# Performance work log

Measured on AMD Instinct MI355X. Metric: run time of the kernel, lower is better.

Reference implementation:

```python
import jax, jax.numpy as jnp
import numpy as np
import math

D_MODEL = 512
NHEAD = 8
N_LAYERS = 3
D_FF = 2048
INPUT_DIM = 128
NUM_CLASSES = 64
FACTOR = 5


def setup_inputs() -> dict:
    key = jax.random.key(0)
    ks = jax.random.split(key, 24)
    s = 0.02
    d, f, nl = D_MODEL, D_FF, N_LAYERS
    inp = {
        "x": jax.random.normal(ks[0], (4, 1024, INPUT_DIM), dtype=jnp.float32),
        "W_emb": jax.random.normal(ks[1], (INPUT_DIM, d), dtype=jnp.float32) * s,
        "b_emb": jnp.zeros((d,), jnp.float32),
        "Wq": jax.random.normal(ks[2], (nl, d, d), dtype=jnp.float32) * s,
        "bq": jnp.zeros((nl, d), jnp.float32),
        "Wk": jax.random.normal(ks[3], (nl, d, d), dtype=jnp.float32) * s,
        "bk": jnp.zeros((nl, d), jnp.float32),
        "Wv": jax.random.normal(ks[4], (nl, d, d), dtype=jnp.float32) * s,
        "bv": jnp.zeros((nl, d), jnp.float32),
        "Wo": jax.random.normal(ks[5], (nl, d, d), dtype=jnp.float32) * s,
        "bo": jnp.zeros((nl, d), jnp.float32),
        "ln1_g": jnp.ones((nl, d), jnp.float32),
        "ln1_b": jnp.zeros((nl, d), jnp.float32),
        "W1": jax.random.normal(ks[6], (nl, d, f), dtype=jnp.float32) * s,
        "b1": jnp.zeros((nl, f), jnp.float32),
        "W2": jax.random.normal(ks[7], (nl, f, d), dtype=jnp.float32) * s,
        "b2": jnp.zeros((nl, d), jnp.float32),
        "ln2_g": jnp.ones((nl, d), jnp.float32),
        "ln2_b": jnp.zeros((nl, d), jnp.float32),
        "W_dec": jax.random.normal(ks[8], (d, NUM_CLASSES), dtype=jnp.float32) * s,
        "b_dec": jnp.zeros((NUM_CLASSES,), jnp.float32),
    }
    return inp


def _layer_norm(x, g, b, eps=1e-5):
    m = jnp.mean(x, axis=-1, keepdims=True)
    v = jnp.var(x, axis=-1, keepdims=True)
    return (x - m) * jax.lax.rsqrt(v + eps) * g + b


def _pos_encoding(L, d):
    pos = jnp.arange(L, dtype=jnp.float32)[:, None]
    div = jnp.exp(jnp.arange(0, d, 2, dtype=jnp.float32) * (-math.log(10000.0) / d))
    pe = jnp.zeros((L, d), jnp.float32)
    pe = pe.at[:, 0::2].set(jnp.sin(pos * div))
    pe = pe.at[:, 1::2].set(jnp.cos(pos * div))
    return pe


def _prob_sparse_attn(x, Wq, bq, Wk, bk, Wv, bv, Wo, bo):
    B, L, d = x.shape
    H, dk = NHEAD, d // NHEAD
    u = min(L, int(FACTOR * math.log(L)) if L > 1 else L)
    Q = (x @ Wq + bq).reshape(B, L, H, dk).transpose(0, 2, 1, 3)  # bhld
    K = (x @ Wk + bk).reshape(B, L, H, dk).transpose(0, 2, 1, 3)
    V = (x @ Wv + bv).reshape(B, L, H, dk).transpose(0, 2, 1, 3)
    scores = jnp.einsum("bhld,bhmd->bhlm", Q, K) / math.sqrt(dk)  # [B,H,L,L]
    kth = jax.lax.top_k(scores, u)[0][..., -1:]  # kth-largest per row
    scores = jnp.where(scores < kth, -10000.0, scores)
    attn = jax.nn.softmax(scores, axis=-1)
    out = jnp.einsum("bhlm,bhmd->bhld", attn, V)
    out = out.transpose(0, 2, 1, 3).reshape(B, L, d)
    return out @ Wo + bo


def reference(x, W_emb, b_emb, Wq, bq, Wk, bk, Wv, bv, Wo, bo,
              ln1_g, ln1_b, W1, b1, W2, b2, ln2_g, ln2_b, W_dec, b_dec):
    B, L, _ = x.shape
    h = (x @ W_emb + b_emb) * math.sqrt(D_MODEL)
    h = h + _pos_encoding(L, D_MODEL)[None]
    for i in range(N_LAYERS):
        a = _prob_sparse_attn(h, Wq[i], bq[i], Wk[i], bk[i], Wv[i], bv[i], Wo[i], bo[i])
        h = _layer_norm(h + a, ln1_g[i], ln1_b[i])
        ff = jax.nn.relu(h @ W1[i] + b1[i]) @ W2[i] + b2[i]
        h = _layer_norm(h + ff, ln2_g[i], ln2_b[i])
    return h @ W_dec + b_dec
```

## Files before the change

### kernel.cpp

```cpp
#include <hip/hip_runtime.h>
#include <math.h>

#define SEQ 1024
#define BATCH 4
#define DMODEL 512
#define NHEAD 8
#define DK 64
#define DFF 2048
#define U_TOP 34
#define ROWS (BATCH * SEQ)

typedef unsigned short ushort_t;
typedef __attribute__((ext_vector_type(8))) short short8;
typedef __attribute__((ext_vector_type(4))) float float4v;

__device__ inline ushort_t f2bf(float f) {
  unsigned u = __float_as_uint(f);
  unsigned r = u + 0x7fffu + ((u >> 16) & 1u);
  return (ushort_t)(r >> 16);
}
__device__ inline float bf2f(ushort_t u) {
  return __uint_as_float((unsigned)u << 16);
}
__device__ inline float keyinv(unsigned cand) {
  unsigned fb = (cand & 0x80000000u) ? (cand ^ 0x80000000u) : ~cand;
  return __uint_as_float(fb);
}

union H16 { _Float16 h; unsigned short u; };
__device__ inline unsigned short h2u(float f) {
  H16 t; t.h = (_Float16)f; return t.u;
}
__device__ inline float u2h(unsigned short u) {
  H16 t; t.u = u; return (float)t.h;
}
__device__ inline int mbcnt64(unsigned long long m) {
  int lo = __builtin_amdgcn_mbcnt_lo((unsigned)m, 0);
  return __builtin_amdgcn_mbcnt_hi((unsigned)(m >> 32), lo);
}

__device__ inline void glds16(const void* g, void* l) {
  __builtin_amdgcn_global_load_lds(
      (const __attribute__((address_space(1))) unsigned int*)g,
      (__attribute__((address_space(3))) unsigned int*)l, 16, 0, 0);
}

__device__ inline void bitonic64x2(float& a, float& b, int lane) {
#pragma unroll
  for (int k = 2; k <= 64; k <<= 1) {
#pragma unroll
    for (int j = k >> 1; j > 0; j >>= 1) {
      float pa = __shfl_xor(a, j);
      float pb = __shfl_xor(b, j);
      bool keepMin = (((lane & k) != 0) == ((lane & j) == 0));
      a = keepMin ? fminf(a, pa) : fmaxf(a, pa);
      b = keepMin ? fminf(b, pb) : fmaxf(b, pb);
    }
  }
}

template <int RELU, int SPLIT>
__global__ __launch_bounds__(256) void gemm128(
    const ushort_t* __restrict__ A, const short* __restrict__ Bt,
    const float* __restrict__ b0, const float* __restrict__ b1,
    const float* __restrict__ b2, ushort_t* __restrict__ Cout,
    int K, int N, int zCstride) {
  __shared__ short As[128 * 32];
  __shared__ short Bs[128 * 32];

  const int tid = threadIdx.x;
  const int lane = tid & 63, w = tid >> 6;
  const int wm = w >> 1, wn = w & 1;
  const int quad = lane >> 4, r16 = lane & 15;
  const int bm = blockIdx.y * 128, bn = blockIdx.x * 128;

  const int srow = lane >> 2, skseg = lane & 3;
  const ushort_t* Ag0 = A + (size_t)(bm + w * 16 + srow) * K + skseg * 8;
  const ushort_t* Ag1 = Ag0 + (size_t)64 * K;
  const short* Bg0 = Bt + (size_t)(bn + w * 16 + srow) * K + skseg * 8;
  const short* Bg1 = Bg0 + (size_t)64 * K;
  short* lA0 = As + (w * 16) * 32;
  short* lA1 = As + (64 + w * 16) * 32;
  short* lB0 = Bs + (w * 16) * 32;
  short* lB1 = Bs + (64 + w * 16) * 32;

  float4v acc[4][4];
#pragma unroll
  for (int m = 0; m < 4; ++m)
#pragma unroll
    for (int n = 0; n < 4; ++n) acc[m][n] = (float4v){0.f, 0.f, 0.f, 0.f};

  for (int k0 = 0; k0 < K; k0 += 32) {
    __syncthreads();
    glds16(Ag0 + k0, lA0);
    glds16(Ag1 + k0, lA1);
    glds16(Bg0 + k0, lB0);
    glds16(Bg1 + k0, lB1);
    __syncthreads();

    short8 af[4], bfr[4];
#pragma unroll
    for (int m = 0; m < 4; ++m)
      af[m] = *(const short8*)&As[(wm * 64 + m * 16 + r16) * 32 + quad * 8];
#pragma unroll
    for (int n = 0; n < 4; ++n)
      bfr[n] = *(const short8*)&Bs[(wn * 64 + n * 16 + r16) * 32 + quad * 8];
#pragma unroll
    for (int m = 0; m < 4; ++m)
#pragma unroll
      for (int n = 0; n < 4; ++n)
        acc[m][n] = __builtin_amdgcn_mfma_f32_16x16x32_bf16(af[m], bfr[n],
                                                            acc[m][n], 0, 0, 0);
  }

  const int z = SPLIT ? (bn >> 9) : 0;
  const float* bias = (z == 0) ? b0 : (z == 1 ? b1 : b2);
  const int cbase = SPLIT ? (bn & 511) : bn;
  const int strideN = SPLIT ? 512 : N;
  ushort_t* C = Cout + (SPLIT ? (size_t)z * zCstride : (size_t)0);

  float bias_n[4];
#pragma unroll
  for (int n = 0; n < 4; ++n)
    bias_n[n] = bias[cbase + wn * 64 + n * 16 + r16];

#pragma unroll
  for (int m = 0; m < 4; ++m) {
#pragma unroll
    for (int n = 0; n < 4; ++n) {
      int col = cbase + wn * 64 + n * 16 + r16;
#pragma unroll
      for (int reg = 0; reg < 4; ++reg) {
        int row = bm + wm * 64 + m * 16 + quad * 4 + reg;
        float v = acc[m][n][reg] + bias_n[n];
        if (RELU) v = fmaxf(v, 0.f);
        C[(size_t)row * strideN + col] = f2bf(v);
      }
    }
  }
}

template <int RELU, int OUTBF16, int EPI, int ADDC>
__global__ __launch_bounds__(256) void gemm64(
    const ushort_t* __restrict__ A, const short* __restrict__ Bt,
    const float* __restrict__ bias, void* __restrict__ Cout,
    const ushort_t* __restrict__ Cadd, int K, int N) {
  __shared__ short As[64 * 32];
  __shared__ short Bs[64 * 32];

  const int tid = threadIdx.x;
  const int lane = tid & 63, w = tid >> 6;
  const int wm = w >> 1, wn = w & 1;
  const int quad = lane >> 4, r16 = lane & 15;
  const int bm = blockIdx.y * 64, bn = blockIdx.x * 64;

  const int srow = tid >> 2, skseg = tid & 3;
  const ushort_t* Ag = A + (size_t)(bm + srow) * K + skseg * 8;
  const short* Bg = Bt + (size_t)(bn + srow) * K + skseg * 8;
  short* lA = As + w * 512;
  short* lB = Bs + w * 512;

  float4v acc[2][2];
#pragma unroll
  for (int m = 0; m < 2; ++m)
#pragma unroll
    for (int n = 0; n < 2; ++n) acc[m][n] = (float4v){0.f, 0.f, 0.f, 0.f};

  for (int k0 = 0; k0 < K; k0 += 32) {
    __syncthreads();
    glds16(Ag + k0, lA);
    glds16(Bg + k0, lB);
    __syncthreads();

    short8 af[2], bfr[2];
#pragma unroll
    for (int m = 0; m < 2; ++m)
      af[m] = *(const short8*)&As[(wm * 32 + m * 16 + r16) * 32 + quad * 8];
#pragma unroll
    for (int n = 0; n < 2; ++n)
      bfr[n] = *(const short8*)&Bs[(wn * 32 + n * 16 + r16) * 32 + quad * 8];
#pragma unroll
    for (int m = 0; m < 2; ++m)
#pragma unroll
      for (int n = 0; n < 2; ++n)
        acc[m][n] = __builtin_amdgcn_mfma_f32_16x16x32_bf16(af[m], bfr[n],
                                                            acc[m][n], 0, 0, 0);
  }

  const float pe_c = (float)(-9.210340371976184 / 512.0);
  const float sqrtd = 22.62741699796952f;

  float bias_n[2];
#pragma unroll
  for (int n = 0; n < 2; ++n) bias_n[n] = bias[bn + wn * 32 + n * 16 + r16];

#pragma unroll
  for (int m = 0; m < 2; ++m) {
#pragma unroll
    for (int n = 0; n < 2; ++n) {
      int col = bn + wn * 32 + n * 16 + r16;
#pragma unroll
      for (int reg = 0; reg < 4; ++reg) {
        int row = bm + wm * 32 + m * 16 + quad * 4 + reg;
        float v = acc[m][n][reg] + bias_n[n];
        if (RELU) v = fmaxf(v, 0.f);
        if (EPI == 2) {
          int pos = row & (SEQ - 1);
          float e = __expf((float)(col & ~1) * pe_c);
          float arg = (float)pos * e;
          v = v * sqrtd + ((col & 1) ? __cosf(arg) : __sinf(arg));
        }
        if (ADDC) v += bf2f(Cadd[(size_t)row * N + col]);
        if (OUTBF16) {
          ((ushort_t*)Cout)[(size_t)row * N + col] = f2bf(v);
        } else {
          ((float*)Cout)[(size_t)row * N + col] = v;
        }
      }
    }
  }
}

__global__ __launch_bounds__(256) void convert_all(
    const float* __restrict__ Wq, const float* __restrict__ Wk,
    const float* __restrict__ Wv, const float* __restrict__ Wo,
    const float* __restrict__ W1, const float* __restrict__ W2,
    const float* __restrict__ W_emb, const float* __restrict__ W_dec,
    short* __restrict__ wt) {
  __shared__ float t[32][33];
  int id = blockIdx.x;
  const float* src;
  short* dst;
  int K, N, tk, tn;
  if (id < 9216) {
    int lay = id / 3072, r = id % 3072;
    short* wl = wt + (size_t)lay * 3145728;
    const size_t wsz = 512 * 512;
    if (r < 1024) {
      int wi = r >> 8, tile = r & 255;
      const float* base = (wi == 0) ? Wq : (wi == 1) ? Wk : (wi == 2) ? Wv : Wo;
      src = base + lay * wsz;
      dst = wl + wi * 262144;
      K = 512; N = 512; tk = tile >> 4; tn = tile & 15;
    } else if (r < 2048) {
      int tile = r - 1024;
      src = W1 + (size_t)lay * 512 * 2048;
      dst = wl + 1048576;
      K = 512; N = 2048; tk = tile >> 6; tn = tile & 63;
    } else {
      int tile = r - 2048;
      src = W2 + (size_t)lay * 2048 * 512;
      dst = wl + 2097152;
      K = 2048; N = 512; tk = tile >> 4; tn = tile & 15;
    }
  } else {
    int r = id - 9216;
    if (r < 64) {
      src = W_emb; dst = wt + 9437184; K = 128; N = 512; tk = r >> 4; tn = r & 15;
    } else {
      r -= 64;
      src = W_dec; dst = wt + 9502720; K = 512; N = 64; tk = r >> 1; tn = r & 1;
    }
  }
  const int k0 = tk * 32, n0 = tn * 32;
  const int tx = threadIdx.x, ty = threadIdx.y;
#pragma unroll
  for (int i = 0; i < 4; ++i) {
    int r = ty + i * 8;
    t[r][tx] = src[(size_t)(k0 + r) * N + n0 + tx];
  }
  __syncthreads();
#pragma unroll
  for (int i = 0; i < 4; ++i) {
    int r = ty + i * 8;
    dst[(size_t)(n0 + r) * K + k0 + tx] = (short)f2bf(t[tx][r]);
  }
}

__global__ __launch_bounds__(256) void f32_to_bf16_kernel(
    const float* __restrict__ src, ushort_t* __restrict__ dst) {
  int i = blockIdx.x * blockDim.x + threadIdx.x;
  float4 v = ((const float4*)src)[i];
  ushort4 o;
  o.x = f2bf(v.x); o.y = f2bf(v.y); o.z = f2bf(v.z); o.w = f2bf(v.w);
  ((ushort4*)dst)[i] = o;
}

__global__ __launch_bounds__(256) void ln_kernel(
    const ushort_t* __restrict__ t1b, const float* __restrict__ g,
    const float* __restrict__ bb, ushort_t* __restrict__ hb) {
  const int row = blockIdx.x * 4 + (threadIdx.x >> 6);
  const int lane = threadIdx.x & 63;
  const size_t base = (size_t)row * DMODEL + lane * 8;
  uint4 raw = *(const uint4*)(t1b + base);
  unsigned rr[4] = {raw.x, raw.y, raw.z, raw.w};
  float v[8];
#pragma unroll
  for (int k = 0; k < 4; ++k) {
    v[2 * k] = bf2f((ushort_t)(rr[k] & 0xffff));
    v[2 * k + 1] = bf2f((ushort_t)(rr[k] >> 16));
  }
  float sum = 0.f, sq = 0.f;
#pragma unroll
  for (int k = 0; k < 8; ++k) { sum += v[k]; sq += v[k] * v[k]; }
#pragma unroll
  for (int off = 32; off; off >>= 1) {
    sum += __shfl_xor(sum, off);
    sq += __shfl_xor(sq, off);
  }
  float mean = sum * (1.f / 512.f);
  float var = fmaxf(sq * (1.f / 512.f) - mean * mean, 0.f);
  float rstd = 1.f / sqrtf(var + 1e-5f);
  float4 g0 = *(const float4*)(g + lane * 8);
  float4 g1 = *(const float4*)(g + lane * 8 + 4);
  float4 c0 = *(const float4*)(bb + lane * 8);
  float4 c1 = *(const float4*)(bb + lane * 8 + 4);
  float gg[8] = {g0.x, g0.y, g0.z, g0.w, g1.x, g1.y, g1.z, g1.w};
  float cc[8] = {c0.x, c0.y, c0.z, c0.w, c1.x, c1.y, c1.z, c1.w};
  uint4 out;
  unsigned* op = (unsigned*)&out;
#pragma unroll
  for (int k = 0; k < 4; ++k) {
    float y0 = (v[2 * k] - mean) * rstd * gg[2 * k] + cc[2 * k];
    float y1 = (v[2 * k + 1] - mean) * rstd * gg[2 * k + 1] + cc[2 * k + 1];
    op[k] = (unsigned)f2bf(y0) | ((unsigned)f2bf(y1) << 16);
  }
  *(uint4*)(hb + base) = out;
}

#define SST 1048

__global__ __launch_bounds__(512, 8) void attn_kernel(
    const ushort_t* __restrict__ Qb, const ushort_t* __restrict__ Kb,
    const ushort_t* __restrict__ Vb, ushort_t* __restrict__ Ob) {
  __shared__ _Float16 s16[16 * SST];
  __shared__ unsigned plist[16][64];

  const int tid = threadIdx.x;
  const int q0 = blockIdx.x * 16;
  const int h = blockIdx.y;
  const int b = blockIdx.z;
  const int w = tid >> 6;
  const int lane = tid & 63;
  const int quad = lane >> 4, r16 = lane & 15;

  {
    const int j0 = w * 128;
    const ushort_t* qrow =
        Qb + (size_t)(b * SEQ + q0 + r16) * DMODEL + h * DK + quad * 8;
    short8 aq0 = *(const short8*)qrow;
    short8 aq1 = *(const short8*)(qrow + 32);

#pragma unroll
    for (int nt = 0; nt < 8; ++nt) {
      const ushort_t* krow =
          Kb + (size_t)(b * SEQ + j0 + nt * 16 + r16) * DMODEL + h * DK +
          quad * 8;
      short8 bk0 = *(const short8*)krow;
      short8 bk1 = *(const short8*)(krow + 32);
      float4v a = (float4v){0.f, 0.f, 0.f, 0.f};
      a = __builtin_amdgcn_mfma_f32_16x16x32_bf16(aq0, bk0, a, 0, 0, 0);
      a = __builtin_amdgcn_mfma_f32_16x16x32_bf16(aq1, bk1, a, 0, 0, 0);
#pragma unroll
      for (int reg = 0; reg < 4; ++reg)
        s16[(quad * 4 + reg) * SST + j0 + nt * 16 + r16] =
            (_Float16)(a[reg] * 0.125f);
    }
  }
  __syncthreads();

  {
    const int qa = w, qb2 = w + 8;
    const _Float16* sa = &s16[qa * SST];
    const _Float16* sb = &s16[qb2 * SST];

    float la = -1e30f, lb = -1e30f;
#pragma unroll
    for (int i = 0; i < 16; ++i) {
      la = fmaxf(la, (float)sa[lane + 64 * i]);
      lb = fmaxf(lb, (float)sb[lane + 64 * i]);
    }

    float sva = la, svb = lb;
    bitonic64x2(sva, svb, lane);
    const float mxa = __shfl(sva, 0), mxb = __shfl(svb, 0);
    const float fTa = __shfl(sva, 33), fTb = __shfl(svb, 33);

    int ca = 0, cb = 0;
#pragma unroll
    for (int i = 0; i < 16; ++i) {
      float va = (float)sa[lane + 64 * i];
      float vb = (float)sb[lane + 64 * i];
      bool ka = va >= fTa, kb = vb >= fTb;
      unsigned long long ma = __ballot(ka);
      unsigned long long mb = __ballot(kb);
      if (ka) {
        int p = ca + mbcnt64(ma);
        if (p < 64)
          plist[qa][p] = ((unsigned)(lane + 64 * i) << 16) |
                         h2u(__expf(va - mxa));
      }
      if (kb) {
        int p = cb + mbcnt64(mb);
        if (p < 64)
          plist[qb2][p] = ((unsigned)(lane + 64 * i) << 16) |
                          h2u(__expf(vb - mxb));
      }
      ca += (int)__popcll(ma);
      cb += (int)__popcll(mb);
    }

    if (__builtin_expect(ca > 64, 0)) {
      unsigned ans = 0u;
      int cge = ca;
      bool ex = false;
      for (int bit = 31; bit >= 0 && cge > 64 && !ex; --bit) {
        unsigned cand = ans | (1u << bit);
        float fc = keyinv(cand);
        int c = 0;
#pragma unroll
        for (int i = 0; i < 16; ++i)
          c += (int)__popcll(__ballot((float)sa[lane + 64 * i] >= fc));
        if (c >= U_TOP) { ans = cand; cge = c; ex = (c == U_TOP); }
      }
      float fa2 = keyinv(ans);
      int cc = 0;
#pragma unroll
      for (int i = 0; i < 16; ++i) {
        float va = (float)sa[lane + 64 * i];
        bool ka = va >= fa2;
        unsigned long long ma = __ballot(ka);
        if (ka) {
          int p = cc + mbcnt64(ma);
          if (p < 64)
            plist[qa][p] = ((unsigned)(lane + 64 * i) << 16) |
                           h2u(__expf(va - mxa));
        }
        cc += (int)__popcll(ma);
      }
      ca = cc;
    }
    if (__builtin_expect(cb > 64, 0)) {
      unsigned ans = 0u;
      int cge = cb;
      bool ex = false;
      for (int bit = 31; bit >= 0 && cge > 64 && !ex; --bit) {
        unsigned cand = ans | (1u << bit);
        float fc = keyinv(cand);
        int c = 0;
#pragma unroll
        for (int i = 0; i < 16; ++i)
          c += (int)__popcll(__ballot((float)sb[lane + 64 * i] >= fc));
        if (c >= U_TOP) { ans = cand; cge = c; ex = (c == U_TOP); }
      }
      float fb2 = keyinv(ans);
      int cc = 0;
#pragma unroll
      for (int i = 0; i < 16; ++i) {
        float vb = (float)sb[lane + 64 * i];
        bool kb = vb >= fb2;
        unsigned long long mb = __ballot(kb);
        if (kb) {
          int p = cc + mbcnt64(mb);
          if (p < 64)
            plist[qb2][p] = ((unsigned)(lane + 64 * i) << 16) |
                            h2u(__expf(vb - mxb));
        }
        cc += (int)__popcll(mb);
      }
      cb = cc;
    }
    ca = ca > 64 ? 64 : ca;
    cb = cb > 64 ? 64 : cb;

    unsigned pua = (lane < ca) ? plist[qa][lane] : 0u;
    unsigned pub = (lane < cb) ? plist[qb2][lane] : 0u;
    float ea = u2h((unsigned short)(pua & 0xffffu));
    float eb = u2h((unsigned short)(pub & 0xffffu));

    float s2a = ea, s2b = eb;
    bitonic64x2(s2a, s2b, lane);
    const float tha = __shfl(s2a, 33), thb = __shfl(s2b, 33);

    bool keepa = ea >= tha, keepb = eb >= thb;
    unsigned long long kma = __ballot(keepa);
    unsigned long long kmb = __ballot(keepb);
    int na = (int)__popcll(kma), nb = (int)__popcll(kmb);
    float za = keepa ? ea : 0.f, zb = keepb ? eb : 0.f;
#pragma unroll
    for (int off = 32; off; off >>= 1) {
      za += __shfl_xor(za, off);
      zb += __shfl_xor(zb, off);
    }
    int posa = mbcnt64(kma), posb = mbcnt64(kmb);
    if (keepa) plist[qa][posa] = pua;
    if (keepb) plist[qb2][posb] = pub;

    const ushort_t* vbase = Vb + (size_t)b * SEQ * DMODEL + h * DK;
    float oa = 0.f, ob = 0.f;
    int nmax = na > nb ? na : nb;
    for (int i = 0; i < nmax; i += 2) {
      unsigned ua0 = (i < na) ? plist[qa][i] : 0u;
      unsigned ua1 = (i + 1 < na) ? plist[qa][i + 1] : 0u;
      unsigned ub0 = (i < nb) ? plist[qb2][i] : 0u;
      unsigned ub1 = (i + 1 < nb) ? plist[qb2][i + 1] : 0u;
      float pa0 = bf2f(vbase[(size_t)(ua0 >> 16) * DMODEL + lane]);
      float pa1 = bf2f(vbase[(size_t)(ua1 >> 16) * DMODEL + lane]);
      float pb0 = bf2f(vbase[(size_t)(ub0 >> 16) * DMODEL + lane]);
      float pb1 = bf2f(vbase[(size_t)(ub1 >> 16) * DMODEL + lane]);
      oa += u2h((unsigned short)(ua0 & 0xffffu)) * pa0 +
            u2h((unsigned short)(ua1 & 0xffffu)) * pa1;
      ob += u2h((unsigned short)(ub0 & 0xffffu)) * pb0 +
            u2h((unsigned short)(ub1 & 0xffffu)) * pb1;
    }
    oa /= za;
    ob /= zb;
    Ob[(size_t)(b * SEQ + q0 + qa) * DMODEL + h * DK + lane] = f2bf(oa);
    Ob[(size_t)(b * SEQ + q0 + qb2) * DMODEL + h * DK + lane] = f2bf(ob);
  }
}

extern "C" void kernel_launch(void* const* d_in, const int* in_sizes, int n_in,
                              void* d_out, int out_size, void* d_ws,
                              size_t ws_size, hipStream_t stream) {
  const float* x = (const float*)d_in[0];
  const float* W_emb = (const float*)d_in[1];
  const float* b_emb = (const float*)d_in[2];
  const float* Wq = (const float*)d_in[3];
  const float* bq = (const float*)d_in[4];
  const float* Wk = (const float*)d_in[5];
  const float* bk = (const float*)d_in[6];
  const float* Wv = (const float*)d_in[7];
  const float* bv = (const float*)d_in[8];
  const float* Wo = (const float*)d_in[9];
  const float* bo = (const float*)d_in[10];
  const float* ln1_g = (const float*)d_in[11];
  const float* ln1_b = (const float*)d_in[12];
  const float* W1 = (const float*)d_in[13];
  const float* b1 = (const float*)d_in[14];
  const float* W2 = (const float*)d_in[15];
  const float* b2 = (const float*)d_in[16];
  const float* ln2_g = (const float*)d_in[17];
  const float* ln2_b = (const float*)d_in[18];
  const float* W_dec = (const float*)d_in[19];
  const float* b_dec = (const float*)d_in[20];

  char* wsb = (char*)d_ws;
  ushort_t* qkv = (ushort_t*)wsb;
  ushort_t* ffh = (ushort_t*)wsb;
  ushort_t* ao = (ushort_t*)(wsb + ((size_t)16 << 20));
  ushort_t* xb = (ushort_t*)(wsb + ((size_t)16 << 20));
  ushort_t* t1b = (ushort_t*)(wsb + ((size_t)20 << 20));
  ushort_t* hb = (ushort_t*)(wsb + ((size_t)24 << 20));
  short* wt = (short*)(wsb + ((size_t)28 << 20));
  short* wembT = wt + 9437184;
  short* wdecT = wt + 9502720;

  f32_to_bf16_kernel<<<dim3(512), 256, 0, stream>>>(x, xb);
  convert_all<<<dim3(9312), dim3(32, 8), 0, stream>>>(Wq, Wk, Wv, Wo, W1, W2,
                                                      W_emb, W_dec, wt);
  gemm64<0, 1, 2, 0><<<dim3(8, 64), 256, 0, stream>>>(
      xb, wembT, b_emb, (void*)hb, nullptr, 128, 512);

  for (int i = 0; i < 3; ++i) {
    short* wtL = wt + (size_t)i * 3145728;

    gemm128<0, 1><<<dim3(12, 32), 256, 0, stream>>>(
        hb, wtL, bq + i * DMODEL, bk + i * DMODEL, bv + i * DMODEL, qkv, 512,
        512, 2097152);

    attn_kernel<<<dim3(SEQ / 16, NHEAD, BATCH), dim3(512), 0, stream>>>(
        qkv, qkv + 2097152, qkv + 4194304, ao);

    gemm64<0, 1, 0, 1><<<dim3(8, 64), 256, 0, stream>>>(
        ao, wtL + 786432, bo + i * DMODEL, (void*)t1b, hb, 512, 512);
    ln_kernel<<<dim3(ROWS / 4), 256, 0, stream>>>(
        t1b, ln1_g + i * DMODEL, ln1_b + i * DMODEL, hb);

    gemm128<1, 0><<<dim3(16, 32), 256, 0, stream>>>(
        hb, wtL + 1048576, b1 + i * DFF, nullptr, nullptr, ffh, 512, 2048, 0);
    gemm64<0, 1, 0, 1><<<dim3(8, 64), 256, 0, stream>>>(
        ffh, wtL + 2097152, b2 + i * DMODEL, (void*)t1b, hb, 2048, 512);
    ln_kernel<<<dim3(ROWS / 4), 256, 0, stream>>>(
        t1b, ln2_g + i * DMODEL, ln2_b + i * DMODEL, hb);
  }

  gemm64<0, 0, 0, 0><<<dim3(1, 64), 256, 0, stream>>>(
      hb, wdecT, b_dec, d_out, nullptr, 512, 64);
}
```

Measured before the change: 564.0 us.

## Split-K the output and FFN2 projections and fuse reduction into LayerNorm

Replaces the 64x64-tile GEMMs for the attention output projection and the second FFN projection with a 128x128-tile split-K GEMM over two K halves. Each half writes a bf16 partial to workspace, and the LayerNorm kernel now sums both partials plus the residual before normalizing. The aim is better MFMA tile efficiency and reuse while keeping the block count near 256, and it removes the separate residual-add epilogue. In exchange it adds an extra partial write and read, and an extra bf16 rounding of each partial, which may cost accuracy.

```diff
diff --git a/kernel.cpp b/kernel.cpp
--- a/kernel.cpp
+++ b/kernel.cpp
@@ -135,6 +135,82 @@
         float v = acc[m][n][reg] + bias_n[n];
         if (RELU) v = fmaxf(v, 0.f);
         C[(size_t)row * strideN + col] = f2bf(v);
+      }
+    }
+  }
+}
+
+__global__ __launch_bounds__(256) void gemm128sk(
+    const ushort_t* __restrict__ A, const short* __restrict__ Bt,
+    const float* __restrict__ bias, ushort_t* __restrict__ pout,
+    int K, int Ks) {
+  __shared__ short As[128 * 32];
+  __shared__ short Bs[128 * 32];
+
+  const int tid = threadIdx.x;
+  const int lane = tid & 63, w = tid >> 6;
+  const int wm = w >> 1, wn = w & 1;
+  const int quad = lane >> 4, r16 = lane & 15;
+  const int bm = blockIdx.y * 128, bn = blockIdx.x * 128;
+  const int z = blockIdx.z;
+  const int koff = z * Ks;
+
+  const int srow = lane >> 2, skseg = lane & 3;
+  const ushort_t* Ag0 =
+      A + (size_t)(bm + w * 16 + srow) * K + skseg * 8 + koff;
+  const ushort_t* Ag1 = Ag0 + (size_t)64 * K;
+  const short* Bg0 = Bt + (size_t)(bn + w * 16 + srow) * K + skseg * 8 + koff;
+  const short* Bg1 = Bg0 + (size_t)64 * K;
+  short* lA0 = As + (w * 16) * 32;
+  short* lA1 = As + (64 + w * 16) * 32;
+  short* lB0 = Bs + (w * 16) * 32;
+  short* lB1 = Bs + (64 + w * 16) * 32;
+
+  float4v acc[4][4];
+#pragma unroll
+  for (int m = 0; m < 4; ++m)
+#pragma unroll
+    for (int n = 0; n < 4; ++n) acc[m][n] = (float4v){0.f, 0.f, 0.f, 0.f};
+
+  for (int k0 = 0; k0 < Ks; k0 += 32) {
+    __syncthreads();
+    glds16(Ag0 + k0, lA0);
+    glds16(Ag1 + k0, lA1);
+    glds16(Bg0 + k0, lB0);
+    glds16(Bg1 + k0, lB1);
+    __syncthreads();
+
+    short8 af[4], bfr[4];
+#pragma unroll
+    for (int m = 0; m < 4; ++m)
+      af[m] = *(const short8*)&As[(wm * 64 + m * 16 + r16) * 32 + quad * 8];
+#pragma unroll
+    for (int n = 0; n < 4; ++n)
+      bfr[n] = *(const short8*)&Bs[(wn * 64 + n * 16 + r16) * 32 + quad * 8];
+#pragma unroll
+    for (int m = 0; m < 4; ++m)
+#pragma unroll
+      for (int n = 0; n < 4; ++n)
+        acc[m][n] = __builtin_amdgcn_mfma_f32_16x16x32_bf16(af[m], bfr[n],
+                                                            acc[m][n], 0, 0, 0);
+  }
+
+  ushort_t* P = pout + (size_t)z * 2097152;
+  float bias_n[4];
+#pragma unroll
+  for (int n = 0; n < 4; ++n)
+    bias_n[n] = (z == 0) ? bias[bn + wn * 64 + n * 16 + r16] : 0.f;
+
+#pragma unroll
+  for (int m = 0; m < 4; ++m) {
+#pragma unroll
+    for (int n = 0; n < 4; ++n) {
+      int col = bn + wn * 64 + n * 16 + r16;
+#pragma unroll
+      for (int reg = 0; reg < 4; ++reg) {
+        int row = bm + wm * 64 + m * 16 + quad * 4 + reg;
+        float v = acc[m][n][reg] + bias_n[n];
+        P[(size_t)row * 512 + col] = f2bf(v);
       }
     }
   }
@@ -286,19 +362,28 @@
   ((ushort4*)dst)[i] = o;
 }
 
-__global__ __launch_bounds__(256) void ln_kernel(
-    const ushort_t* __restrict__ t1b, const float* __restrict__ g,
-    const float* __restrict__ bb, ushort_t* __restrict__ hb) {
+__global__ __launch_bounds__(256) void ln_red_kernel(
+    const ushort_t* __restrict__ pa, const ushort_t* __restrict__ pb,
+    const float* __restrict__ g, const float* __restrict__ bb,
+    ushort_t* __restrict__ hb) {
   const int row = blockIdx.x * 4 + (threadIdx.x >> 6);
   const int lane = threadIdx.x & 63;
   const size_t base = (size_t)row * DMODEL + lane * 8;
-  uint4 raw = *(const uint4*)(t1b + base);
-  unsigned rr[4] = {raw.x, raw.y, raw.z, raw.w};
+  uint4 ra = *(const uint4*)(pa + base);
+  uint4 rb = *(const uint4*)(pb + base);
+  uint4 rh = *(const uint4*)(hb + base);
+  unsigned aa[4] = {ra.x, ra.y, ra.z, ra.w};
+  unsigned ab[4] = {rb.x, rb.y, rb.z, rb.w};
+  unsigned ah[4] = {rh.x, rh.y, rh.z, rh.w};
   float v[8];
 #pragma unroll
   for (int k = 0; k < 4; ++k) {
-    v[2 * k] = bf2f((ushort_t)(rr[k] & 0xffff));
-    v[2 * k + 1] = bf2f((ushort_t)(rr[k] >> 16));
+    v[2 * k] = bf2f((ushort_t)(aa[k] & 0xffff)) +
+               bf2f((ushort_t)(ab[k] & 0xffff)) +
+               bf2f((ushort_t)(ah[k] & 0xffff));
+    v[2 * k + 1] = bf2f((ushort_t)(aa[k] >> 16)) +
+                   bf2f((ushort_t)(ab[k] >> 16)) +
+                   bf2f((ushort_t)(ah[k] >> 16));
   }
   float sum = 0.f, sq = 0.f;
 #pragma unroll
@@ -548,9 +633,10 @@
   char* wsb = (char*)d_ws;
   ushort_t* qkv = (ushort_t*)wsb;
   ushort_t* ffh = (ushort_t*)wsb;
+  ushort_t* wop = (ushort_t*)wsb;
   ushort_t* ao = (ushort_t*)(wsb + ((size_t)16 << 20));
   ushort_t* xb = (ushort_t*)(wsb + ((size_t)16 << 20));
-  ushort_t* t1b = (ushort_t*)(wsb + ((size_t)20 << 20));
+  ushort_t* ffp = (ushort_t*)(wsb + ((size_t)16 << 20));
   ushort_t* hb = (ushort_t*)(wsb + ((size_t)24 << 20));
   short* wt = (short*)(wsb + ((size_t)28 << 20));
   short* wembT = wt + 9437184;
@@ -572,17 +658,17 @@
     attn_kernel<<<dim3(SEQ / 16, NHEAD, BATCH), dim3(512), 0, stream>>>(
         qkv, qkv + 2097152, qkv + 4194304, ao);
 
-    gemm64<0, 1, 0, 1><<<dim3(8, 64), 256, 0, stream>>>(
-        ao, wtL + 786432, bo + i * DMODEL, (void*)t1b, hb, 512, 512);
-    ln_kernel<<<dim3(ROWS / 4), 256, 0, stream>>>(
-        t1b, ln1_g + i * DMODEL, ln1_b + i * DMODEL, hb);
+    gemm128sk<<<dim3(4, 32, 2), 256, 0, stream>>>(
+        ao, wtL + 786432, bo + i * DMODEL, wop, 512, 256);
+    ln_red_kernel<<<dim3(ROWS / 4), 256, 0, stream>>>(
+        wop, wop + 2097152, ln1_g + i * DMODEL, ln1_b + i * DMODEL, hb);
 
     gemm128<1, 0><<<dim3(16, 32), 256, 0, stream>>>(
         hb, wtL + 1048576, b1 + i * DFF, nullptr, nullptr, ffh, 512, 2048, 0);
-    gemm64<0, 1, 0, 1><<<dim3(8, 64), 256, 0, stream>>>(
-        ffh, wtL + 2097152, b2 + i * DMODEL, (void*)t1b, hb, 2048, 512);
-    ln_kernel<<<dim3(ROWS / 4), 256, 0, stream>>>(
-        t1b, ln2_g + i * DMODEL, ln2_b + i * DMODEL, hb);
+    gemm128sk<<<dim3(4, 32, 2), 256, 0, stream>>>(
+        ffh, wtL + 2097152, b2 + i * DMODEL, ffp, 2048, 1024);
+    ln_red_kernel<<<dim3(ROWS / 4), 256, 0, stream>>>(
+        ffp, ffp + 2097152, ln2_g + i * DMODEL, ln2_b + i * DMODEL, hb);
   }
 
   gemm64<0, 0, 0, 0><<<dim3(1, 64), 256, 0, stream>>>(
```

Measured after the change: 558.1 us. No clear change (-1.0%).
